# Optimization experiments

Measured on AMD Instinct MI355X. Metric: run time of the kernel, lower is better.

## Reference

```python
import jax, jax.numpy as jnp
import numpy as np

B, M, L, LQ, E, V = 32, 100, 30, 30, 256, 32000


def position_encoding(seq_len, emb):
    # faithful to MemN2N position encoding: 1 + 4*(k - (E+1)/2)*(j - (J+1)/2)/(E*J)
    j = jnp.arange(1, seq_len + 1, dtype=jnp.float32)[:, None]   # (J,1)
    k = jnp.arange(1, emb + 1, dtype=jnp.float32)[None, :]       # (1,E)
    half_e = (emb + 1) / 2.0
    half_j = (seq_len + 1) / 2.0
    return 1.0 + 4.0 * (k - half_e) * (j - half_j) / (emb * seq_len)  # (J,E)


def masked_softmax(x, m):
    xm = jnp.where(m > 0, x, -1e30)
    e = jnp.exp(xm - jnp.max(xm, axis=-1, keepdims=True)) * m
    return e / (jnp.sum(e, axis=-1, keepdims=True) + 1e-13)


def masked_log_softmax(x, m):
    return jax.nn.log_softmax(x + jnp.log(m + 1e-13), axis=-1)


def _forward(trainS, trainQ, trainVM, trainPM, trainSM, trainQM,
             A1, A2, A3, A4, W, b, gamma, beta):
    # query encoding: embed + position encode + query mask + sum over words
    Q = trainQ[:, 0, :]                                   # (B,LQ)
    pe_q = position_encoding(LQ, E)                       # (LQ,E)
    u = jnp.sum(A1[Q] * pe_q * trainQM[:, :, None], axis=1)  # (B,E)

    # story memory embeddings: gather + PE + sum over words.
    # NOTE: original code multiplies by trainSM but discards the result (bug),
    # so SM is intentionally NOT applied here.
    pe_s = position_encoding(L, E)                        # (L,E)
    embA1 = jnp.sum(A1[trainS] * pe_s, axis=2)            # (B,M,E)
    embA2 = jnp.sum(A2[trainS] * pe_s, axis=2)
    embA3 = jnp.sum(A3[trainS] * pe_s, axis=2)
    embA4 = jnp.sum(A4[trainS] * pe_s, axis=2)

    def hop(memA, memC, u):
        # scores = sum_E(memA * u) * PM (PM applied pre-sum is equivalent)
        scores = jnp.einsum('bme,be->bm', memA, u) * trainPM
        p = masked_softmax(scores, trainPM)               # (B,M)
        o = jnp.einsum('bm,bme->be', p, memC)             # (B,E)
        return o + u

    u = hop(embA1, embA2, u)   # hop 1
    u = hop(embA2, embA3, u)   # hop 2
    u = hop(embA3, embA4, u)   # hop 3

    # final linear + BatchNorm1d (training-mode batch stats, eps=1e-5)
    wx = u @ W.T + b                                      # (B,V)
    mean = jnp.mean(wx, axis=0)
    var = jnp.mean((wx - mean) ** 2, axis=0)
    y = gamma * (wx - mean) / jnp.sqrt(var + 1e-5) + beta
    return masked_log_softmax(y, trainVM)


def setup_inputs() -> dict:
    key = jax.random.key(0)
    ks = jax.random.split(key, 8)
    inp = {
        'trainS': jax.random.randint(ks[0], (B, M, L), 0, V, dtype=jnp.int32),
        'trainQ': jax.random.randint(ks[1], (B, 1, LQ), 0, V, dtype=jnp.int32),
        'trainVM': jnp.ones((B, V), jnp.float32),
        'trainPM': jnp.ones((B, M), jnp.float32),
        'trainSM': jnp.ones((B, M, L), jnp.float32),
        'trainQM': jnp.ones((B, LQ), jnp.float32),
        'A1': 0.1 * jax.random.normal(ks[2], (V, E), jnp.float32),
        'A2': 0.1 * jax.random.normal(ks[3], (V, E), jnp.float32),
        'A3': 0.1 * jax.random.normal(ks[4], (V, E), jnp.float32),
        'A4': 0.1 * jax.random.normal(ks[5], (V, E), jnp.float32),
        'W': jax.random.normal(ks[6], (V, E), jnp.float32) / np.sqrt(E),
        'b': jnp.zeros((V,), jnp.float32),
        'gamma': jnp.ones((V,), jnp.float32),
        'beta': jnp.zeros((V,), jnp.float32),
        'inspect': 0,
    }
    return inp


def reference(trainS, trainQ, trainVM, trainPM, trainSM, trainQM,
              A1, A2, A3, A4, W, b, gamma, beta, inspect):
    return _forward(trainS, trainQ, trainVM, trainPM, trainSM, trainQM,
                    A1, A2, A3, A4, W, b, gamma, beta)
```

## Files before the change

### kernel.cpp

```cpp
#include <hip/hip_runtime.h>
#include <math.h>

static constexpr int B_ = 32, M_ = 100, L_ = 30, LQ_ = 30, E_ = 256, V_ = 32000;

__global__ __launch_bounds__(256) void k_embed(const int* __restrict__ trainS,
                                               const float* __restrict__ A1,
                                               const float* __restrict__ A2,
                                               const float* __restrict__ A3,
                                               const float* __restrict__ A4,
                                               float* __restrict__ embA) {
    const int bm = blockIdx.x;
    const int tbl = threadIdx.x >> 6;
    const int e0 = (threadIdx.x & 63) * 4;
    const float* __restrict__ A = (tbl == 0) ? A1 : (tbl == 1) ? A2 : (tbl == 2) ? A3 : A4;
    const float half_e = (E_ + 1) * 0.5f;
    const float half_j = (L_ + 1) * 0.5f;
    const float inv = 1.0f / (float)(E_ * L_);
    const float k0 = (float)(e0 + 1) - half_e;
    const float k1 = k0 + 1.f, k2 = k0 + 2.f, k3 = k0 + 3.f;

    int idx[L_];
#pragma unroll
    for (int l = 0; l < L_; ++l) idx[l] = trainS[bm * L_ + l];

    float4 acc = make_float4(0.f, 0.f, 0.f, 0.f);
#pragma unroll
    for (int c = 0; c < 3; ++c) {
        float4 r[10];
#pragma unroll
        for (int j = 0; j < 10; ++j)
            r[j] = *reinterpret_cast<const float4*>(A + (size_t)idx[c * 10 + j] * E_ + e0);
#pragma unroll
        for (int j = 0; j < 10; ++j) {
            const int l = c * 10 + j;
            const float coef = 4.0f * ((float)(l + 1) - half_j) * inv;
            acc.x += r[j].x * (1.0f + coef * k0);
            acc.y += r[j].y * (1.0f + coef * k1);
            acc.z += r[j].z * (1.0f + coef * k2);
            acc.w += r[j].w * (1.0f + coef * k3);
        }
    }
    *reinterpret_cast<float4*>(embA + (size_t)tbl * (B_ * M_ * E_) + (size_t)bm * E_ + e0) = acc;
}

__global__ __launch_bounds__(1024) void k_hops(const int* __restrict__ trainQ,
                                               const float* __restrict__ trainQM,
                                               const float* __restrict__ A1,
                                               const float* __restrict__ embA,
                                               const float* __restrict__ trainPM,
                                               float* __restrict__ u_out) {
    const int b = blockIdx.x;
    const int tid = threadIdx.x;
    const int lane = tid & 63;
    const int wave = tid >> 6;
    const int g = tid >> 8;
    const int e = tid & 255;
    __shared__ float u_sh[E_];
    __shared__ float sc[M_];
    __shared__ float p_sh[M_];
    __shared__ float osum[4][E_];

    {
        const float half_e = (E_ + 1) * 0.5f;
        const float half_j = (LQ_ + 1) * 0.5f;
        const float inv = 1.0f / (float)(E_ * LQ_);
        const float ke = (float)(e + 1) - half_e;
        const int l0 = g * 8;
        const int ln = (LQ_ - l0 < 8) ? (LQ_ - l0) : 8;
        int qi[8];
        float qm[8];
#pragma unroll
        for (int j = 0; j < 8; ++j) {
            if (j < ln) {
                qi[j] = trainQ[b * LQ_ + l0 + j];
                qm[j] = trainQM[b * LQ_ + l0 + j];
            } else { qi[j] = 0; qm[j] = 0.f; }
        }
        float r[8];
#pragma unroll
        for (int j = 0; j < 8; ++j)
            r[j] = (j < ln) ? A1[(size_t)qi[j] * E_ + e] : 0.f;
        float part = 0.f;
#pragma unroll
        for (int j = 0; j < 8; ++j) {
            const float pe = 1.0f + 4.0f * ke * ((float)(l0 + j + 1) - half_j) * inv;
            part += r[j] * pe * qm[j];
        }
        osum[g][e] = part;
    }
    __syncthreads();
    if (tid < E_) u_sh[tid] = osum[0][tid] + osum[1][tid] + osum[2][tid] + osum[3][tid];
    __syncthreads();

    for (int hop = 0; hop < 3; ++hop) {
        const float* memA = embA + (size_t)hop * (B_ * M_ * E_) + (size_t)b * M_ * E_;
        const float* memC = memA + (size_t)(B_ * M_ * E_);
#pragma unroll 2
        for (int m = wave; m < M_; m += 16) {
            const float* row = memA + m * E_;
            float part = 0.f;
#pragma unroll
            for (int j = 0; j < 4; ++j)
                part += row[lane + 64 * j] * u_sh[lane + 64 * j];
#pragma unroll
            for (int off = 32; off > 0; off >>= 1)
                part += __shfl_xor(part, off, 64);
            if (lane == 0) sc[m] = part * trainPM[b * M_ + m];
        }
        __syncthreads();
        if (wave == 0) {
            const float pm0 = (lane < M_) ? trainPM[b * M_ + lane] : 0.f;
            const float pm1 = (lane + 64 < M_) ? trainPM[b * M_ + lane + 64] : 0.f;
            const float x0 = (lane < M_ && pm0 > 0.f) ? sc[lane] : -1e30f;
            const float x1 = (lane + 64 < M_ && pm1 > 0.f) ? sc[lane + 64] : -1e30f;
            float mx = fmaxf(x0, x1);
#pragma unroll
            for (int off = 32; off > 0; off >>= 1)
                mx = fmaxf(mx, __shfl_xor(mx, off, 64));
            const float e0v = (lane < M_) ? expf(x0 - mx) * pm0 : 0.f;
            const float e1v = (lane + 64 < M_) ? expf(x1 - mx) * pm1 : 0.f;
            float ssum = e0v + e1v;
#pragma unroll
            for (int off = 32; off > 0; off >>= 1)
                ssum += __shfl_xor(ssum, off, 64);
            const float invs = 1.0f / (ssum + 1e-13f);
            if (lane < M_) p_sh[lane] = e0v * invs;
            if (lane + 64 < M_) p_sh[lane + 64] = e1v * invs;
        }
        __syncthreads();
        {
            float acc = 0.f;
            const float* crow = memC + e;
            const int m0 = g * 25;
#pragma unroll 5
            for (int mm = 0; mm < 25; ++mm)
                acc += p_sh[m0 + mm] * crow[(size_t)(m0 + mm) * E_];
            osum[g][e] = acc;
        }
        __syncthreads();
        if (tid < E_) u_sh[tid] += osum[0][tid] + osum[1][tid] + osum[2][tid] + osum[3][tid];
        __syncthreads();
    }
    if (tid < E_) u_out[b * E_ + tid] = u_sh[tid];
}

__global__ __launch_bounds__(256) void k_output(const float* __restrict__ u,
                                                const float* __restrict__ Wm,
                                                const float* __restrict__ bias,
                                                const float* __restrict__ gamma,
                                                const float* __restrict__ beta,
                                                const float* __restrict__ VM,
                                                float* __restrict__ z) {
    __shared__ float u_sh[B_ * E_];
    __shared__ float part[128 * 33];
    const int tid = threadIdx.x;
    for (int i = tid; i < (B_ * E_) / 4; i += 256)
        reinterpret_cast<float4*>(u_sh)[i] = reinterpret_cast<const float4*>(u)[i];
    __syncthreads();
    const int vl = tid & 127;
    const int eh = tid >> 7;
    const int v = blockIdx.x * 128 + vl;
    float acc[B_];
#pragma unroll
    for (int b = 0; b < B_; ++b) acc[b] = 0.f;
    const float4* wrow = reinterpret_cast<const float4*>(Wm + (size_t)v * E_ + eh * 128);
#pragma unroll
    for (int c = 0; c < 4; ++c) {
        float4 wb[8];
#pragma unroll
        for (int j = 0; j < 8; ++j) wb[j] = wrow[c * 8 + j];
#pragma unroll
        for (int j = 0; j < 8; ++j) {
            const int e4 = eh * 128 + (c * 8 + j) * 4;
#pragma unroll
            for (int b = 0; b < B_; ++b) {
                const float4 uu = *reinterpret_cast<const float4*>(u_sh + b * E_ + e4);
                acc[b] += wb[j].x * uu.x + wb[j].y * uu.y + wb[j].z * uu.z + wb[j].w * uu.w;
            }
        }
    }
    if (eh == 1) {
#pragma unroll
        for (int b = 0; b < B_; ++b) part[vl * 33 + b] = acc[b];
    }
    __syncthreads();
    if (eh == 0) {
        float wx[B_];
        const float bv = bias[v];
        float mean = 0.f;
#pragma unroll
        for (int b = 0; b < B_; ++b) {
            wx[b] = acc[b] + part[vl * 33 + b] + bv;
            mean += wx[b];
        }
        mean *= (1.0f / B_);
        float var = 0.f;
#pragma unroll
        for (int b = 0; b < B_; ++b) {
            const float d = wx[b] - mean;
            var += d * d;
        }
        var *= (1.0f / B_);
        const float rstd = rsqrtf(var + 1e-5f);
        const float g = gamma[v], be = beta[v];
#pragma unroll
        for (int b = 0; b < B_; ++b) {
            const float y = g * (wx[b] - mean) * rstd + be;
            z[(size_t)b * V_ + v] = y + logf(VM[(size_t)b * V_ + v] + 1e-13f);
        }
    }
}

__global__ __launch_bounds__(256) void k_lsep(const float* __restrict__ z,
                                              float* __restrict__ partial) {
    const int b = blockIdx.x >> 3;
    const int k = blockIdx.x & 7;
    const int tid = threadIdx.x;
    const float4* zr = reinterpret_cast<const float4*>(z + (size_t)b * V_ + k * 4000);
    float s = 0.f;
    for (int i = tid; i < 1000; i += 256) {
        const float4 x = zr[i];
        s += expf(x.x) + expf(x.y) + expf(x.z) + expf(x.w);
    }
#pragma unroll
    for (int off = 32; off > 0; off >>= 1)
        s += __shfl_xor(s, off, 64);
    __shared__ float ss[4];
    const int wave = tid >> 6, lane = tid & 63;
    if (lane == 0) ss[wave] = s;
    __syncthreads();
    if (tid == 0) partial[blockIdx.x] = ss[0] + ss[1] + ss[2] + ss[3];
}

__global__ __launch_bounds__(256) void k_final(const float* __restrict__ z,
                                               const float* __restrict__ partial,
                                               float* __restrict__ out) {
    const int idx = blockIdx.x * 256 + threadIdx.x;
    const int b = idx / (V_ / 4);
    const int v4 = idx % (V_ / 4);
    float s = 0.f;
#pragma unroll
    for (int k = 0; k < 8; ++k) s += partial[b * 8 + k];
    const float lse = logf(s);
    const float4 x = reinterpret_cast<const float4*>(z + (size_t)b * V_)[v4];
    float4 o;
    o.x = x.x - lse; o.y = x.y - lse; o.z = x.z - lse; o.w = x.w - lse;
    reinterpret_cast<float4*>(out + (size_t)b * V_)[v4] = o;
}

extern "C" void kernel_launch(void* const* d_in, const int* in_sizes, int n_in,
                              void* d_out, int out_size, void* d_ws, size_t ws_size,
                              hipStream_t stream) {
    const int* trainS = (const int*)d_in[0];
    const int* trainQ = (const int*)d_in[1];
    const float* trainVM = (const float*)d_in[2];
    const float* trainPM = (const float*)d_in[3];
    const float* trainQM = (const float*)d_in[5];
    const float* A1 = (const float*)d_in[6];
    const float* A2 = (const float*)d_in[7];
    const float* A3 = (const float*)d_in[8];
    const float* A4 = (const float*)d_in[9];
    const float* Wm = (const float*)d_in[10];
    const float* bias = (const float*)d_in[11];
    const float* gamma = (const float*)d_in[12];
    const float* beta = (const float*)d_in[13];
    float* out = (float*)d_out;

    float* ws = (float*)d_ws;
    float* u = ws;
    float* embA = ws + 8192;
    float* z = embA + 4 * (B_ * M_ * E_);
    float* partial = z + (size_t)B_ * V_;

    k_embed<<<B_ * M_, 256, 0, stream>>>(trainS, A1, A2, A3, A4, embA);
    k_hops<<<B_, 1024, 0, stream>>>(trainQ, trainQM, A1, embA, trainPM, u);
    k_output<<<V_ / 128, 256, 0, stream>>>(u, Wm, bias, gamma, beta, trainVM, z);
    k_lsep<<<B_ * 8, 256, 0, stream>>>(z, partial);
    k_final<<<(B_ * V_ / 4) / 256, 256, 0, stream>>>(z, partial, out);
}
```

Before: 123.0 us.

## Transpose query state and drop shared-memory staging in output GEMV

The hops kernel now writes the final query vector transposed (E×B), so the output kernel can read all batch values for each embedding element as contiguous float4 loads straight from global/L1. Each thread then computes a full vocabulary row with no shared-memory staging, split-E partial sums or block sync, and the grid is halved to 125 blocks. Separately, the embedding gather now issues 15 loads per batch instead of 10, with a scheduling barrier to keep them grouped. The output kernel occupies fewer CUs, and each thread's W row reads are strided by a full row across lanes, which may coalesce poorly.

```diff
diff --git a/kernel.cpp b/kernel.cpp
--- a/kernel.cpp
+++ b/kernel.cpp
@@ -25,14 +25,15 @@
 
     float4 acc = make_float4(0.f, 0.f, 0.f, 0.f);
 #pragma unroll
-    for (int c = 0; c < 3; ++c) {
-        float4 r[10];
-#pragma unroll
-        for (int j = 0; j < 10; ++j)
-            r[j] = *reinterpret_cast<const float4*>(A + (size_t)idx[c * 10 + j] * E_ + e0);
-#pragma unroll
-        for (int j = 0; j < 10; ++j) {
-            const int l = c * 10 + j;
+    for (int c = 0; c < 2; ++c) {
+        float4 r[15];
+#pragma unroll
+        for (int j = 0; j < 15; ++j)
+            r[j] = *reinterpret_cast<const float4*>(A + (size_t)idx[c * 15 + j] * E_ + e0);
+        __builtin_amdgcn_sched_barrier(0);
+#pragma unroll
+        for (int j = 0; j < 15; ++j) {
+            const int l = c * 15 + j;
             const float coef = 4.0f * ((float)(l + 1) - half_j) * inv;
             acc.x += r[j].x * (1.0f + coef * k0);
             acc.y += r[j].y * (1.0f + coef * k1);
@@ -48,7 +49,7 @@
                                                const float* __restrict__ A1,
                                                const float* __restrict__ embA,
                                                const float* __restrict__ trainPM,
-                                               float* __restrict__ u_out) {
+                                               float* __restrict__ u_T) {
     const int b = blockIdx.x;
     const int tid = threadIdx.x;
     const int lane = tid & 63;
@@ -141,73 +142,61 @@
         if (tid < E_) u_sh[tid] += osum[0][tid] + osum[1][tid] + osum[2][tid] + osum[3][tid];
         __syncthreads();
     }
-    if (tid < E_) u_out[b * E_ + tid] = u_sh[tid];
-}
-
-__global__ __launch_bounds__(256) void k_output(const float* __restrict__ u,
+    if (tid < E_) u_T[tid * B_ + b] = u_sh[tid];
+}
+
+__global__ __launch_bounds__(256) void k_output(const float* __restrict__ u_T,
                                                 const float* __restrict__ Wm,
                                                 const float* __restrict__ bias,
                                                 const float* __restrict__ gamma,
                                                 const float* __restrict__ beta,
                                                 const float* __restrict__ VM,
                                                 float* __restrict__ z) {
-    __shared__ float u_sh[B_ * E_];
-    __shared__ float part[128 * 33];
-    const int tid = threadIdx.x;
-    for (int i = tid; i < (B_ * E_) / 4; i += 256)
-        reinterpret_cast<float4*>(u_sh)[i] = reinterpret_cast<const float4*>(u)[i];
-    __syncthreads();
-    const int vl = tid & 127;
-    const int eh = tid >> 7;
-    const int v = blockIdx.x * 128 + vl;
+    const int v = blockIdx.x * 256 + threadIdx.x;
+    const float* __restrict__ wr = Wm + (size_t)v * E_;
     float acc[B_];
 #pragma unroll
     for (int b = 0; b < B_; ++b) acc[b] = 0.f;
-    const float4* wrow = reinterpret_cast<const float4*>(Wm + (size_t)v * E_ + eh * 128);
-#pragma unroll
-    for (int c = 0; c < 4; ++c) {
+
+#pragma unroll
+    for (int c = 0; c < 8; ++c) {
         float4 wb[8];
 #pragma unroll
-        for (int j = 0; j < 8; ++j) wb[j] = wrow[c * 8 + j];
+        for (int j = 0; j < 8; ++j)
+            wb[j] = reinterpret_cast<const float4*>(wr)[c * 8 + j];
 #pragma unroll
         for (int j = 0; j < 8; ++j) {
-            const int e4 = eh * 128 + (c * 8 + j) * 4;
-#pragma unroll
-            for (int b = 0; b < B_; ++b) {
-                const float4 uu = *reinterpret_cast<const float4*>(u_sh + b * E_ + e4);
-                acc[b] += wb[j].x * uu.x + wb[j].y * uu.y + wb[j].z * uu.z + wb[j].w * uu.w;
+#pragma unroll
+            for (int eo = 0; eo < 4; ++eo) {
+                const float we = (eo == 0) ? wb[j].x : (eo == 1) ? wb[j].y : (eo == 2) ? wb[j].z : wb[j].w;
+                const float* __restrict__ ur = u_T + (c * 32 + j * 4 + eo) * B_;
+#pragma unroll
+                for (int b4 = 0; b4 < 8; ++b4) {
+                    const float4 ub = *reinterpret_cast<const float4*>(ur + b4 * 4);
+                    acc[b4 * 4 + 0] += we * ub.x;
+                    acc[b4 * 4 + 1] += we * ub.y;
+                    acc[b4 * 4 + 2] += we * ub.z;
+                    acc[b4 * 4 + 3] += we * ub.w;
+                }
             }
         }
     }
-    if (eh == 1) {
-#pragma unroll
-        for (int b = 0; b < B_; ++b) part[vl * 33 + b] = acc[b];
-    }
-    __syncthreads();
-    if (eh == 0) {
-        float wx[B_];
-        const float bv = bias[v];
-        float mean = 0.f;
-#pragma unroll
-        for (int b = 0; b < B_; ++b) {
-            wx[b] = acc[b] + part[vl * 33 + b] + bv;
-            mean += wx[b];
-        }
-        mean *= (1.0f / B_);
-        float var = 0.f;
-#pragma unroll
-        for (int b = 0; b < B_; ++b) {
-            const float d = wx[b] - mean;
-            var += d * d;
-        }
-        var *= (1.0f / B_);
-        const float rstd = rsqrtf(var + 1e-5f);
-        const float g = gamma[v], be = beta[v];
-#pragma unroll
-        for (int b = 0; b < B_; ++b) {
-            const float y = g * (wx[b] - mean) * rstd + be;
-            z[(size_t)b * V_ + v] = y + logf(VM[(size_t)b * V_ + v] + 1e-13f);
-        }
+
+    const float bv = bias[v];
+    float mean = 0.f;
+#pragma unroll
+    for (int b = 0; b < B_; ++b) { acc[b] += bv; mean += acc[b]; }
+    mean *= (1.0f / B_);
+    float var = 0.f;
+#pragma unroll
+    for (int b = 0; b < B_; ++b) { const float d = acc[b] - mean; var += d * d; }
+    var *= (1.0f / B_);
+    const float rstd = rsqrtf(var + 1e-5f);
+    const float g = gamma[v], be = beta[v];
+#pragma unroll
+    for (int b = 0; b < B_; ++b) {
+        const float y = g * (acc[b] - mean) * rstd + be;
+        z[(size_t)b * V_ + v] = y + logf(VM[(size_t)b * V_ + v] + 1e-13f);
     }
 }
 
@@ -267,14 +256,14 @@
     float* out = (float*)d_out;
 
     float* ws = (float*)d_ws;
-    float* u = ws;
+    float* u_T = ws;
     float* embA = ws + 8192;
     float* z = embA + 4 * (B_ * M_ * E_);
     float* partial = z + (size_t)B_ * V_;
 
     k_embed<<<B_ * M_, 256, 0, stream>>>(trainS, A1, A2, A3, A4, embA);
-    k_hops<<<B_, 1024, 0, stream>>>(trainQ, trainQM, A1, embA, trainPM, u);
-    k_output<<<V_ / 128, 256, 0, stream>>>(u, Wm, bias, gamma, beta, trainVM, z);
+    k_hops<<<B_, 1024, 0, stream>>>(trainQ, trainQM, A1, embA, trainPM, u_T);
+    k_output<<<V_ / 256, 256, 0, stream>>>(u_T, Wm, bias, gamma, beta, trainVM, z);
     k_lsep<<<B_ * 8, 256, 0, stream>>>(z, partial);
     k_final<<<(B_ * V_ / 4) / 256, 256, 0, stream>>>(z, partial, out);
 }
```

After: 168.9 us. 1.37x slower.
